# Kernel optimization log

Measured on AMD Instinct MI355X. Metric: run time of the kernel, lower is better.

Reference implementation:

```python
import jax, jax.numpy as jnp
import numpy as np

HP = 64  # padded height (next pow2 of 56)
WP = 64  # padded width
H, W = 56, 56


def fwht(x):
    """Walsh-Hadamard transform along last axis (n must be power of 2)."""
    n = x.shape[-1]
    h = 1
    while h < n:
        xr = x.reshape(*x.shape[:-1], n // (2 * h), 2 * h)
        a = xr[..., :h]
        b = xr[..., h:]
        x = jnp.concatenate([a + b, a - b], axis=-1).reshape(*x.shape[:-1], n)
        h *= 2
    return x


def fwht_axis(x, axis):
    if axis == -1:
        return fwht(x)
    return jnp.swapaxes(fwht(jnp.swapaxes(x, -1, axis)), -1, axis)


def ifwht_axis(x, axis):
    n = x.shape[axis]
    return fwht_axis(x, axis) / n


def setup_inputs() -> dict:
    key = jax.random.key(0)
    k1, k2, k3, k4 = jax.random.split(key, 4)
    x = jax.random.normal(k1, (64, 128, H, W), dtype=jnp.float32)
    # per-pod 1x1 conv weights (pods, out_ch, in_ch), kaiming-ish scale
    conv_w = jax.random.normal(k2, (2, 128, 128), dtype=jnp.float32) / np.sqrt(128.0)
    v = jax.random.uniform(k3, (2, HP, WP), dtype=jnp.float32)
    T = jax.random.uniform(k4, (2, HP, WP), dtype=jnp.float32) / 10.0
    return {"x": x, "conv_w": conv_w, "v": v, "T": T}


def reference(x, conv_w, v, T):
    # pad spatial dims to power of 2 (pad right/bottom)
    f0 = jnp.pad(x, ((0, 0), (0, 0), (0, HP - H), (0, WP - W)))
    # 2D WHT
    f1 = fwht_axis(f0, -1)
    f2 = fwht_axis(f1, -2)
    # per-pod: elementwise gate v, 1x1 conv, soft-threshold; then sum over pods
    # f3: (P, B, Cin, HP, WP)
    f3 = v[:, None, None, :, :] * f2[None]
    f4 = jnp.einsum('pbihw,poi->pbohw', f3, conv_w)
    thr = jax.nn.relu(T)[:, None, None, :, :]
    f5 = jnp.sign(f4) * jax.nn.relu(jnp.abs(f4) - thr)
    f6 = f5.sum(axis=0)
    # inverse 2D WHT
    f7 = ifwht_axis(f6, -1)
    f8 = ifwht_axis(f7, -2)
    y = f8[..., :H, :W]
    return y + x  # residual
```

## Files before the change

### kernel.cpp

```cpp
#include <hip/hip_runtime.h>

typedef unsigned short u16;
typedef unsigned int u32;
typedef __attribute__((ext_vector_type(8))) __bf16 bf16x8;
typedef __attribute__((ext_vector_type(8))) unsigned short u16x8;
typedef __attribute__((ext_vector_type(2))) unsigned int u32x2;
typedef __attribute__((ext_vector_type(4))) float f32x4;

__device__ __forceinline__ u16 f2bf(float f) {
  u32 u = __builtin_bit_cast(u32, f);
  u += 0x7FFFu + ((u >> 16) & 1u);
  return (u16)(u >> 16);
}
__device__ __forceinline__ float bf2f(u16 h) {
  u32 u = ((u32)h) << 16;
  return __builtin_bit_cast(float, u);
}

template <int M>
__device__ __forceinline__ void bfly16(float r[16]) {
#pragma unroll
  for (int j = 0; j < 16; ++j)
    if ((j & M) == 0) {
      float a = r[j], b = r[j | M];
      r[j] = a + b;
      r[j | M] = a - b;
    }
}
template <int M>
__device__ __forceinline__ void bfly64(float r[64]) {
#pragma unroll
  for (int j = 0; j < 64; ++j)
    if ((j & M) == 0) {
      float a = r[j], b = r[j | M];
      r[j] = a + b;
      r[j | M] = a - b;
    }
}

__global__ __launch_bounds__(256) void k0_wcat(const float* __restrict__ cw,
                                               u16* __restrict__ wc) {
  const int i = blockIdx.x * 256 + threadIdx.x;
  const int j = i & 7;
  const int lr = (i >> 3) & 15;
  const int lq = (i >> 7) & 3;
  const int q = (i >> 9) & 3;
  const int fm = (i >> 11) & 1;
  const int wv = (i >> 12) & 3;
  const int fp = (i >> 14) & 1;
  const int row = fp * 128 + wv * 32 + fm * 16 + lr;
  const int k = q * 32 + lq * 8 + j;
  wc[i] = f2bf(cw[row * 128 + k]);
}

__global__ __launch_bounds__(512) void k1_fwht(const float* __restrict__ x,
                                               u16* __restrict__ f2) {
  __shared__ u16 lo[4096 * 8];
  const int t = threadIdx.x;
  const int w = t & 63;
  const int p = t >> 6;
  const int b = blockIdx.x >> 4;
  const int cg = blockIdx.x & 15;
  const float* xp = x + (size_t)(b * 128 + cg * 8 + p) * 3136;

  float r[64];
#pragma unroll
  for (int h = 56; h < 64; ++h) r[h] = 0.f;
  if (w < 56) {
#pragma unroll
    for (int h = 0; h < 56; ++h) r[h] = xp[h * 56 + w];
  } else {
#pragma unroll
    for (int h = 0; h < 56; ++h) r[h] = 0.f;
  }

  bfly64<1>(r); bfly64<2>(r); bfly64<4>(r); bfly64<8>(r);
  bfly64<16>(r); bfly64<32>(r);

#define K1_WST(M)                                    \
  {                                                  \
    _Pragma("unroll") for (int h = 0; h < 64; ++h) { \
      const float v = __shfl_xor(r[h], M, 64);       \
      r[h] = (w & M) ? (v - r[h]) : (r[h] + v);      \
    }                                                \
  }
  K1_WST(1) K1_WST(2) K1_WST(4) K1_WST(8) K1_WST(16) K1_WST(32)
#undef K1_WST

#pragma unroll
  for (int h = 0; h < 64; ++h) lo[(h * 64 + w) * 8 + p] = f2bf(r[h]);
  __syncthreads();

  u16* dst = f2 + ((size_t)(b * 16 + cg) << 15);
#pragma unroll
  for (int k = 0; k < 8; ++k) {
    const int g = k * 512 + t;
    *(u16x8*)(dst + (size_t)g * 8) = *(const u16x8*)&lo[g * 8];
  }
}

__global__ __launch_bounds__(256, 2) void k2_mix(u16* __restrict__ fg,
                                                 const u16* __restrict__ wc,
                                                 const float* __restrict__ vv,
                                                 const float* __restrict__ tt) {
  const int t = threadIdx.x;
  const int b = blockIdx.x >> 6;
  const int p0 = (blockIdx.x & 63) << 6;
  u16* fb = fg + ((size_t)b << 19);
  const int wv = t >> 6, l = t & 63, lr = l & 15, lq = l >> 4;

  bf16x8 bfr[4][4];
#pragma unroll
  for (int q = 0; q < 4; ++q)
#pragma unroll
    for (int fn = 0; fn < 4; ++fn)
      bfr[q][fn] = __builtin_bit_cast(
          bf16x8, *(const u16x8*)(fb + ((size_t)(4 * q + lq) << 15) +
                                  (size_t)(p0 + fn * 16 + lr) * 8));
  bf16x8 afr[4][2][2];
#pragma unroll
  for (int q = 0; q < 4; ++q)
#pragma unroll
    for (int fp = 0; fp < 2; ++fp)
#pragma unroll
      for (int fm = 0; fm < 2; ++fm) {
        const int frag_id = ((fp * 4 + wv) * 2 + fm) * 4 + q;
        afr[q][fp][fm] = __builtin_bit_cast(
            bf16x8, *(const u16x8*)(wc + (frag_id << 9) + l * 8));
      }
  float v0s[4], v1s[4], t0s[4], t1s[4];
#pragma unroll
  for (int fn = 0; fn < 4; ++fn) {
    const int pos = p0 + fn * 16 + lr;
    v0s[fn] = vv[pos];
    v1s[fn] = vv[4096 + pos];
    t0s[fn] = fmaxf(tt[pos], 0.f);
    t1s[fn] = fmaxf(tt[4096 + pos], 0.f);
  }

  f32x4 acc[2][2][4] = {};
#pragma unroll
  for (int q = 0; q < 4; ++q)
#pragma unroll
    for (int fn = 0; fn < 4; ++fn)
#pragma unroll
      for (int fp = 0; fp < 2; ++fp)
#pragma unroll
        for (int fm = 0; fm < 2; ++fm)
          acc[fp][fm][fn] = __builtin_amdgcn_mfma_f32_16x16x32_bf16(
              afr[q][fp][fm], bfr[q][fn], acc[fp][fm][fn], 0, 0, 0);

  __syncthreads();
#pragma unroll
  for (int fn = 0; fn < 4; ++fn) {
    const int pos = p0 + fn * 16 + lr;
#pragma unroll
    for (int fm = 0; fm < 2; ++fm) {
      u16 w[4];
#pragma unroll
      for (int rg = 0; rg < 4; ++rg) {
        const float z0 = v0s[fn] * acc[0][fm][fn][rg];
        const float z1 = v1s[fn] * acc[1][fm][fn][rg];
        const float s0v = copysignf(fmaxf(fabsf(z0) - t0s[fn], 0.f), z0);
        const float s1v = copysignf(fmaxf(fabsf(z1) - t1s[fn], 0.f), z1);
        w[rg] = f2bf(s0v + s1v);
      }
      const int og = wv * 4 + fm * 2 + (lq >> 1);
      u32x2 pk;
      pk[0] = (u32)w[0] | ((u32)w[1] << 16);
      pk[1] = (u32)w[2] | ((u32)w[3] << 16);
      *(u32x2*)(fb + ((size_t)og << 15) + (size_t)pos * 8 + (lq & 1) * 4) = pk;
    }
  }
}

__global__ __launch_bounds__(256) void k3_iwht(const u16* __restrict__ g,
                                               const float* __restrict__ x,
                                               float* __restrict__ y) {
  __shared__ float lds[64 * 68];
  const int t = threadIdx.x;
  const int b = blockIdx.x >> 4;
  const int og = blockIdx.x & 15;
  const u16* gb = g + ((size_t)(b * 16 + og) << 15);
  const int hA = t >> 2, wq = t & 3;
  const int hg = t >> 4, rB = t & 15;
  const int wC = t & 63, rr = t >> 6;
  u16x8 inv[16];
#pragma unroll
  for (int e = 0; e < 16; ++e)
    inv[e] = *(const u16x8*)(gb + (size_t)(hA * 64 + wq * 16 + e) * 8);

#pragma unroll
  for (int pp = 0; pp < 8; ++pp) {
    float r[16];
#pragma unroll
    for (int e = 0; e < 16; ++e) r[e] = bf2f(inv[e][pp]);
    bfly16<1>(r); bfly16<2>(r); bfly16<4>(r); bfly16<8>(r);
    if (pp) __syncthreads();
#pragma unroll
    for (int c4 = 0; c4 < 4; ++c4)
      *(float4*)&lds[hA * 68 + wq * 16 + c4 * 4] =
          make_float4(r[c4 * 4 + 0], r[c4 * 4 + 1], r[c4 * 4 + 2], r[c4 * 4 + 3]);
    __syncthreads();
    float q[16];
#pragma unroll
    for (int k = 0; k < 4; ++k)
#pragma unroll
      for (int d = 0; d < 4; ++d)
        q[k * 4 + d] = lds[(hg * 4 + d) * 68 + k * 16 + rB];
    bfly16<4>(q); bfly16<8>(q); bfly16<1>(q); bfly16<2>(q);
#pragma unroll
    for (int k = 0; k < 4; ++k)
#pragma unroll
      for (int d = 0; d < 4; ++d)
        lds[(hg * 4 + d) * 68 + k * 16 + rB] = q[k * 4 + d];
    __syncthreads();
    float s[16];
#pragma unroll
    for (int j = 0; j < 16; ++j) s[j] = lds[(4 * j + rr) * 68 + wC];
    bfly16<1>(s); bfly16<2>(s); bfly16<4>(s); bfly16<8>(s);
    if (wC < 56) {
      const size_t plane = (size_t)(b * 128 + og * 8 + pp) * 3136;
#pragma unroll
      for (int j = 0; j < 14; ++j) {
        const int h = 4 * j + rr;
        const size_t idx = plane + (size_t)(h * 56 + wC);
        y[idx] = x[idx] + s[j] * (1.f / 4096.f);
      }
    }
  }
}

extern "C" void kernel_launch(void* const* d_in, const int* in_sizes, int n_in,
                              void* d_out, int out_size, void* d_ws, size_t ws_size,
                              hipStream_t stream) {
  const float* x = (const float*)d_in[0];
  const float* cw = (const float*)d_in[1];
  const float* v = (const float*)d_in[2];
  const float* T = (const float*)d_in[3];
  float* y = (float*)d_out;

  u16* f2 = (u16*)d_ws;
  u16* wcat = (u16*)((char*)d_ws + 67108864);

  k0_wcat<<<128, 256, 0, stream>>>(cw, wcat);
  k1_fwht<<<1024, 512, 0, stream>>>(x, f2);
  k2_mix<<<4096, 256, 0, stream>>>(f2, wcat, v, T);
  k3_iwht<<<1024, 256, 0, stream>>>(f2, x, y);
}
```

Before: 133.2 us.

## Compute forward 2D Walsh-Hadamard transform with bf16 MFMA matmuls

Replaces the register butterfly and cross-lane shuffle forward WHT with two 64x64 matrix multiplies against a Hadamard matrix built in registers, run on bf16 MFMA. The first product's result is transposed through a per-wave LDS tile before the second. Input loads become float4 row reads. This removes the many VALU and shuffle operations, but it rounds the input and the intermediate to bf16, which costs accuracy, and it raises LDS use.

```diff
diff --git a/kernel.cpp b/kernel.cpp
--- a/kernel.cpp
+++ b/kernel.cpp
@@ -21,16 +21,6 @@
 __device__ __forceinline__ void bfly16(float r[16]) {
 #pragma unroll
   for (int j = 0; j < 16; ++j)
-    if ((j & M) == 0) {
-      float a = r[j], b = r[j | M];
-      r[j] = a + b;
-      r[j | M] = a - b;
-    }
-}
-template <int M>
-__device__ __forceinline__ void bfly64(float r[64]) {
-#pragma unroll
-  for (int j = 0; j < 64; ++j)
     if ((j & M) == 0) {
       float a = r[j], b = r[j | M];
       r[j] = a + b;
@@ -53,49 +43,112 @@
   wc[i] = f2bf(cw[row * 128 + k]);
 }
 
-__global__ __launch_bounds__(512) void k1_fwht(const float* __restrict__ x,
-                                               u16* __restrict__ f2) {
-  __shared__ u16 lo[4096 * 8];
+__global__ __launch_bounds__(512, 2) void k1_fwht(const float* __restrict__ x,
+                                                  u16* __restrict__ f2) {
+  __shared__ u16 c1t[8][64 * 72];
+  __shared__ u16 ostg[4096 * 8];
   const int t = threadIdx.x;
-  const int w = t & 63;
   const int p = t >> 6;
-  const int b = blockIdx.x >> 4;
-  const int cg = blockIdx.x & 15;
+  const int l = t & 63, lr = l & 15, lq = l >> 4;
+  const int b = blockIdx.x >> 4, cg = blockIdx.x & 15;
   const float* xp = x + (size_t)(b * 128 + cg * 8 + p) * 3136;
 
-  float r[64];
-#pragma unroll
-  for (int h = 56; h < 64; ++h) r[h] = 0.f;
-  if (w < 56) {
-#pragma unroll
-    for (int h = 0; h < 56; ++h) r[h] = xp[h * 56 + w];
-  } else {
-#pragma unroll
-    for (int h = 0; h < 56; ++h) r[h] = 0.f;
-  }
-
-  bfly64<1>(r); bfly64<2>(r); bfly64<4>(r); bfly64<8>(r);
-  bfly64<16>(r); bfly64<32>(r);
-
-#define K1_WST(M)                                    \
-  {                                                  \
-    _Pragma("unroll") for (int h = 0; h < 64; ++h) { \
-      const float v = __shfl_xor(r[h], M, 64);       \
-      r[h] = (w & M) ? (v - r[h]) : (r[h] + v);      \
-    }                                                \
-  }
-  K1_WST(1) K1_WST(2) K1_WST(4) K1_WST(8) K1_WST(16) K1_WST(32)
-#undef K1_WST
-
-#pragma unroll
-  for (int h = 0; h < 64; ++h) lo[(h * 64 + w) * 8 + p] = f2bf(r[h]);
+  u16x8 hf[4][2];
+#pragma unroll
+  for (int tl = 0; tl < 4; ++tl)
+#pragma unroll
+    for (int q = 0; q < 2; ++q)
+#pragma unroll
+      for (int j = 0; j < 8; ++j) {
+        const int kk = 32 * q + 8 * lq + j;
+        const int rr = 16 * tl + lr;
+        hf[tl][q][j] = (__builtin_popcount(kk & rr) & 1) ? 0xBF80u : 0x3F80u;
+      }
+
+  float4 xlo[4][2], xhi[4][2];
+#pragma unroll
+  for (int m = 0; m < 4; ++m)
+#pragma unroll
+    for (int q = 0; q < 2; ++q) {
+      const int h = m * 16 + lr;
+      const int w0 = 32 * q + 8 * lq;
+      float4 a = make_float4(0.f, 0.f, 0.f, 0.f);
+      float4 c = make_float4(0.f, 0.f, 0.f, 0.f);
+      if (h < 56 && w0 < 56) {
+        a = *(const float4*)(xp + h * 56 + w0);
+        c = *(const float4*)(xp + h * 56 + w0 + 4);
+      }
+      xlo[m][q] = a;
+      xhi[m][q] = c;
+    }
+  bf16x8 ax[4][2];
+#pragma unroll
+  for (int m = 0; m < 4; ++m)
+#pragma unroll
+    for (int q = 0; q < 2; ++q) {
+      u16x8 v;
+      v[0] = f2bf(xlo[m][q].x); v[1] = f2bf(xlo[m][q].y);
+      v[2] = f2bf(xlo[m][q].z); v[3] = f2bf(xlo[m][q].w);
+      v[4] = f2bf(xhi[m][q].x); v[5] = f2bf(xhi[m][q].y);
+      v[6] = f2bf(xhi[m][q].z); v[7] = f2bf(xhi[m][q].w);
+      ax[m][q] = __builtin_bit_cast(bf16x8, v);
+    }
+
+  f32x4 acc1[4][4] = {};
+#pragma unroll
+  for (int q = 0; q < 2; ++q)
+#pragma unroll
+    for (int m = 0; m < 4; ++m)
+#pragma unroll
+      for (int n = 0; n < 4; ++n)
+        acc1[m][n] = __builtin_amdgcn_mfma_f32_16x16x32_bf16(
+            ax[m][q], __builtin_bit_cast(bf16x8, hf[n][q]), acc1[m][n], 0, 0, 0);
+
+  u16* cwv = &c1t[p][0];
+#pragma unroll
+  for (int m = 0; m < 4; ++m)
+#pragma unroll
+    for (int n = 0; n < 4; ++n) {
+      u32x2 pk;
+      pk[0] = (u32)f2bf(acc1[m][n][0]) | ((u32)f2bf(acc1[m][n][1]) << 16);
+      pk[1] = (u32)f2bf(acc1[m][n][2]) | ((u32)f2bf(acc1[m][n][3]) << 16);
+      *(u32x2*)&cwv[(n * 16 + lr) * 72 + m * 16 + 4 * lq] = pk;
+    }
+
+  bf16x8 cb[4][2];
+#pragma unroll
+  for (int n = 0; n < 4; ++n)
+#pragma unroll
+    for (int q = 0; q < 2; ++q)
+      cb[n][q] = __builtin_bit_cast(
+          bf16x8, *(const u16x8*)&cwv[(n * 16 + lr) * 72 + 32 * q + 8 * lq]);
+
+  f32x4 acc2[4][4] = {};
+#pragma unroll
+  for (int q = 0; q < 2; ++q)
+#pragma unroll
+    for (int m = 0; m < 4; ++m)
+#pragma unroll
+      for (int n = 0; n < 4; ++n)
+        acc2[m][n] = __builtin_amdgcn_mfma_f32_16x16x32_bf16(
+            __builtin_bit_cast(bf16x8, hf[m][q]), cb[n][q], acc2[m][n], 0, 0, 0);
+
+#pragma unroll
+  for (int m = 0; m < 4; ++m)
+#pragma unroll
+    for (int n = 0; n < 4; ++n)
+#pragma unroll
+      for (int r = 0; r < 4; ++r) {
+        const int pos = (m * 16 + 4 * lq + r) * 64 + n * 16 + lr;
+        ostg[pos * 8 + p] = f2bf(acc2[m][n][r]);
+      }
   __syncthreads();
 
   u16* dst = f2 + ((size_t)(b * 16 + cg) << 15);
 #pragma unroll
   for (int k = 0; k < 8; ++k) {
     const int g = k * 512 + t;
-    *(u16x8*)(dst + (size_t)g * 8) = *(const u16x8*)&lo[g * 8];
+    *(u16x8*)(dst + (size_t)g * 8) = *(const u16x8*)&ostg[g * 8];
   }
 }
 
```

Result: faster. 126.9 us (-4.8%).
